# Kernel tuning notes

Measured on AMD Instinct MI355X. Metric: run time of the kernel, lower is better.

## Reference

```python
import jax, jax.numpy as jnp
import numpy as np

DIM = 192
HEADS = 6
WIN = 7


def conv2d(x, w, b, pad):
    # x: (N,C,H,W), w: (O,I,kh,kw)
    y = jax.lax.conv_general_dilated(
        x, w, window_strides=(1, 1), padding=[(pad, pad), (pad, pad)],
        dimension_numbers=('NCHW', 'OIHW', 'NCHW'))
    return y + b[None, :, None, None]


def setup_inputs() -> dict:
    key = jax.random.key(0)
    ks = jax.random.split(key, 4)
    B, C, H, W = 8, DIM, 128, 128
    D = C // HEADS
    s = lambda fan_in: 1.0 / np.sqrt(fan_in)
    return {
        'x': jax.random.normal(ks[0], (B, C, H, W), jnp.float32),
        'w_qkv': jax.random.normal(ks[1], (3 * C, C, 1, 1), jnp.float32) * s(C),
        'b_qkv': jnp.zeros((3 * C,), jnp.float32),
        'w_attn': jax.random.normal(ks[2], (WIN * WIN, 2 * D, WIN, WIN), jnp.float32) * s(2 * D * WIN * WIN),
        'b_attn': jnp.zeros((WIN * WIN,), jnp.float32),
        'w_proj': jax.random.normal(ks[3], (C, C, 1, 1), jnp.float32) * s(C),
        'b_proj': jnp.zeros((C,), jnp.float32),
    }


def reference(x, w_qkv, b_qkv, w_attn, b_attn, w_proj, b_proj):
    B, C, H, W = x.shape
    D = C // HEADS
    scale = D ** -0.5
    # qkv 1x1 conv -> (B, 3, heads, D, H, W)
    qkv = conv2d(x, w_qkv, b_qkv, 0).reshape(B, 3, HEADS, D, H, W)
    q, v = qkv[:, 0], qkv[:, 2]  # NOTE: original code uses q twice (not k)
    q_flat = q.reshape(B * HEADS, D, H, W)
    qq = jnp.concatenate([q_flat * scale, q_flat], axis=1)  # (B*heads, 2D, H, W)
    # conv-generated local attention logits over winSize^2 positions
    attn = conv2d(qq, w_attn, b_attn, WIN // 2)
    attn = jax.nn.softmax(attn, axis=1).reshape(B, HEADS, WIN * WIN, H, W)
    # sum over window dim of v (broadcast over k) * attn (broadcast over d)
    out = jnp.einsum('bhkxy,bhdxy->bhdxy', attn, v).reshape(B, C, H, W)
    return conv2d(out, w_proj, b_proj, 0)
```

## Files before the change

### kernel.cpp

```cpp
#include <hip/hip_runtime.h>
#include <stdint.h>
#include <stddef.h>


#define CDIM 192
#define HWPX 16384
#define LDS_STRIDE 200

typedef __attribute__((ext_vector_type(8))) short short8;
typedef __attribute__((ext_vector_type(4))) float floatx4;
typedef __attribute__((ext_vector_type(4))) unsigned short ushort4_t;

__device__ __forceinline__ unsigned short f2bf(float f) {
    union { float f; unsigned int u; } v; v.f = f;
    unsigned int r = (v.u + 0x7FFFu + ((v.u >> 16) & 1u)) >> 16;
    return (unsigned short)r;
}

__global__ __launch_bounds__(192) void prep_kernel(
    const float* __restrict__ w_qkv, const float* __restrict__ b_qkv,
    const float* __restrict__ w_proj, const float* __restrict__ b_proj,
    unsigned short* __restrict__ Mb, float* __restrict__ bias)
{
    const int o = blockIdx.x, c = threadIdx.x;
    const float* wpr = w_proj + o * CDIM;
    const float* wv  = w_qkv + 2 * CDIM * CDIM;
    float acc = 0.f;
    #pragma unroll 32
    for (int k = 0; k < CDIM; ++k)
        acc = fmaf(wpr[k], wv[k * CDIM + c], acc);
    Mb[o * CDIM + c] = f2bf(acc);

    __shared__ float red[CDIM];
    red[c] = wpr[c] * b_qkv[2 * CDIM + c];
    __syncthreads();
    if (c < 64) {
        float v = red[c] + red[c + 64] + red[c + 128];
        #pragma unroll
        for (int off = 32; off > 0; off >>= 1) v += __shfl_down(v, off);
        if (c == 0) bias[o] = v + b_proj[o];
    }
}

__global__ __launch_bounds__(256, 2) void fused_kernel(
    const float* __restrict__ x,
    const unsigned short* __restrict__ Mb,
    const float* __restrict__ bias,
    float* __restrict__ out)
{
    __shared__ unsigned short Xl[64 * LDS_STRIDE];

    const int tid = threadIdx.x;
    const int bid = blockIdx.x;
    const int b   = bid >> 8;
    const int p0  = (bid & 255) << 6;

    const int lane = tid & 63;
    const int w    = tid >> 6;
    const int n    = lane & 15;
    const int q    = lane >> 4;

    const float* xb = x + (size_t)b * CDIM * HWPX + p0;
    #pragma unroll
    for (int it = 0; it < 3; ++it) {
        const int slot = it * 256 + tid;
        const int p4   = slot & 15;
        const int cg4  = slot >> 4;
        const float* src = xb + (size_t)(cg4 * 4) * HWPX + p4 * 4;
        floatx4 f0 = *(const floatx4*)(src);
        floatx4 f1 = *(const floatx4*)(src + HWPX);
        floatx4 f2 = *(const floatx4*)(src + 2 * HWPX);
        floatx4 f3 = *(const floatx4*)(src + 3 * HWPX);
        #pragma unroll
        for (int i = 0; i < 4; ++i) {
            ushort4_t v4;
            v4.x = f2bf(f0[i]); v4.y = f2bf(f1[i]);
            v4.z = f2bf(f2[i]); v4.w = f2bf(f3[i]);
            *(ushort4_t*)&Xl[(p4 * 4 + i) * LDS_STRIDE + cg4 * 4] = v4;
        }
    }
    __syncthreads();

    floatx4 acc[3][4];
    #pragma unroll
    for (int t = 0; t < 3; ++t)
        #pragma unroll
        for (int pt = 0; pt < 4; ++pt)
            acc[t][pt] = (floatx4){0.f, 0.f, 0.f, 0.f};

    #pragma unroll
    for (int t = 0; t < 3; ++t) {
        const int ot = w * 3 + t;
        short8 a[6];
        const unsigned short* arow = Mb + (ot * 16 + n) * CDIM + q * 8;
        #pragma unroll
        for (int ks = 0; ks < 6; ++ks)
            a[ks] = *(const short8*)(arow + ks * 32);
        #pragma unroll
        for (int pt = 0; pt < 4; ++pt) {
            const unsigned short* brow = &Xl[(pt * 16 + n) * LDS_STRIDE + q * 8];
            #pragma unroll
            for (int ks = 0; ks < 6; ++ks) {
                short8 bfr = *(const short8*)(brow + ks * 32);
                acc[t][pt] = __builtin_amdgcn_mfma_f32_16x16x32_bf16(
                    a[ks], bfr, acc[t][pt], 0, 0, 0);
            }
        }
    }

    float* ob = out + (size_t)b * CDIM * HWPX + p0;
    #pragma unroll
    for (int t = 0; t < 3; ++t) {
        const int ot = w * 3 + t;
        #pragma unroll
        for (int r = 0; r < 4; ++r) {
            const int o = ot * 16 + q * 4 + r;
            const float bo = bias[o];
            float* orow = ob + (size_t)o * HWPX + n;
            #pragma unroll
            for (int pt = 0; pt < 4; ++pt)
                orow[pt * 16] = acc[t][pt][r] + bo;
        }
    }
}

extern "C" void kernel_launch(void* const* d_in, const int* in_sizes, int n_in,
                              void* d_out, int out_size, void* d_ws, size_t ws_size,
                              hipStream_t stream) {
    const float* x      = (const float*)d_in[0];
    const float* w_qkv  = (const float*)d_in[1];
    const float* b_qkv  = (const float*)d_in[2];
    const float* w_proj = (const float*)d_in[5];
    const float* b_proj = (const float*)d_in[6];
    float* out = (float*)d_out;

    unsigned short* Mb = (unsigned short*)d_ws;
    float* bias = (float*)((char*)d_ws + CDIM * CDIM * sizeof(unsigned short));

    const int B = in_sizes[0] / (CDIM * HWPX);

    prep_kernel<<<CDIM, CDIM, 0, stream>>>(w_qkv, b_qkv, w_proj, b_proj, Mb, bias);
    fused_kernel<<<B * 256, 256, 0, stream>>>(x, Mb, bias, out);
}
```

Baseline: 203.4 us.

## Store X in MFMA fragment layout and split work across 8 waves

The fused GEMM kernel now stages x in LDS directly in the MFMA B-fragment order, so each lane reads one short8 with no padded-stride addressing. The block doubles to 512 threads, and the 8 waves split the 64-pixel tile into 2 pixel halves by 4 output-channel groups, each holding all A fragments in registers. The global load pattern changes to per-lane strided scalar loads across channels, which may be less coalesced than the old float4 loads. The prep kernel also gains four independent accumulators to break the FMA dependency chain.

```diff
diff --git a/kernel.cpp b/kernel.cpp
--- a/kernel.cpp
+++ b/kernel.cpp
@@ -5,16 +5,13 @@
 
 #define CDIM 192
 #define HWPX 16384
-#define LDS_STRIDE 200
 
 typedef __attribute__((ext_vector_type(8))) short short8;
 typedef __attribute__((ext_vector_type(4))) float floatx4;
-typedef __attribute__((ext_vector_type(4))) unsigned short ushort4_t;
 
 __device__ __forceinline__ unsigned short f2bf(float f) {
     union { float f; unsigned int u; } v; v.f = f;
-    unsigned int r = (v.u + 0x7FFFu + ((v.u >> 16) & 1u)) >> 16;
-    return (unsigned short)r;
+    return (unsigned short)((v.u + 0x7FFFu + ((v.u >> 16) & 1u)) >> 16);
 }
 
 __global__ __launch_bounds__(192) void prep_kernel(
@@ -25,11 +22,15 @@
     const int o = blockIdx.x, c = threadIdx.x;
     const float* wpr = w_proj + o * CDIM;
     const float* wv  = w_qkv + 2 * CDIM * CDIM;
-    float acc = 0.f;
-    #pragma unroll 32
-    for (int k = 0; k < CDIM; ++k)
-        acc = fmaf(wpr[k], wv[k * CDIM + c], acc);
-    Mb[o * CDIM + c] = f2bf(acc);
+    float a0 = 0.f, a1 = 0.f, a2 = 0.f, a3 = 0.f;
+    #pragma unroll 12
+    for (int k = 0; k < CDIM; k += 4) {
+        a0 = fmaf(wpr[k + 0], wv[(k + 0) * CDIM + c], a0);
+        a1 = fmaf(wpr[k + 1], wv[(k + 1) * CDIM + c], a1);
+        a2 = fmaf(wpr[k + 2], wv[(k + 2) * CDIM + c], a2);
+        a3 = fmaf(wpr[k + 3], wv[(k + 3) * CDIM + c], a3);
+    }
+    Mb[o * CDIM + c] = f2bf((a0 + a1) + (a2 + a3));
 
     __shared__ float red[CDIM];
     red[c] = wpr[c] * b_qkv[2 * CDIM + c];
@@ -42,84 +43,83 @@
     }
 }
 
-__global__ __launch_bounds__(256, 2) void fused_kernel(
+__global__ __launch_bounds__(512, 4) void fused_kernel(
     const float* __restrict__ x,
     const unsigned short* __restrict__ Mb,
     const float* __restrict__ bias,
     float* __restrict__ out)
 {
-    __shared__ unsigned short Xl[64 * LDS_STRIDE];
+    __shared__ short8 Xl[24 * 64];
 
-    const int tid = threadIdx.x;
-    const int bid = blockIdx.x;
-    const int b   = bid >> 8;
-    const int p0  = (bid & 255) << 6;
+    const int tid  = threadIdx.x;
+    const int bid  = blockIdx.x;
+    const int b    = bid >> 8;
+    const int p0   = (bid & 255) << 6;
 
     const int lane = tid & 63;
-    const int w    = tid >> 6;
+    const int wv8  = tid >> 6;
     const int n    = lane & 15;
     const int q    = lane >> 4;
 
     const float* xb = x + (size_t)b * CDIM * HWPX + p0;
     #pragma unroll
-    for (int it = 0; it < 3; ++it) {
-        const int slot = it * 256 + tid;
-        const int p4   = slot & 15;
-        const int cg4  = slot >> 4;
-        const float* src = xb + (size_t)(cg4 * 4) * HWPX + p4 * 4;
-        floatx4 f0 = *(const floatx4*)(src);
-        floatx4 f1 = *(const floatx4*)(src + HWPX);
-        floatx4 f2 = *(const floatx4*)(src + 2 * HWPX);
-        floatx4 f3 = *(const floatx4*)(src + 3 * HWPX);
+    for (int i = 0; i < 3; ++i) {
+        const int f  = i * 8 + wv8;
+        const int pt = f / 6, ks = f % 6;
+        const float* src = xb + (size_t)(ks * 32 + q * 8) * HWPX + (pt * 16 + n);
+        float v[8];
         #pragma unroll
-        for (int i = 0; i < 4; ++i) {
-            ushort4_t v4;
-            v4.x = f2bf(f0[i]); v4.y = f2bf(f1[i]);
-            v4.z = f2bf(f2[i]); v4.w = f2bf(f3[i]);
-            *(ushort4_t*)&Xl[(p4 * 4 + i) * LDS_STRIDE + cg4 * 4] = v4;
-        }
+        for (int j = 0; j < 8; ++j) v[j] = src[(size_t)j * HWPX];
+        short8 fr;
+        #pragma unroll
+        for (int j = 0; j < 8; ++j) fr[j] = (short)f2bf(v[j]);
+        Xl[f * 64 + lane] = fr;
     }
     __syncthreads();
 
-    floatx4 acc[3][4];
+    const int w2 = wv8 & 3;
+    const int wp = wv8 >> 2;
+
+    short8 a[3][6];
+    #pragma unroll
+    for (int t = 0; t < 3; ++t) {
+        const unsigned short* ab = Mb + (size_t)((w2 * 3 + t) * 16 + n) * CDIM + q * 8;
+        #pragma unroll
+        for (int ks = 0; ks < 6; ++ks)
+            a[t][ks] = *(const short8*)(ab + ks * 32);
+    }
+
+    floatx4 acc[3][2];
     #pragma unroll
     for (int t = 0; t < 3; ++t)
         #pragma unroll
-        for (int pt = 0; pt < 4; ++pt)
-            acc[t][pt] = (floatx4){0.f, 0.f, 0.f, 0.f};
+        for (int ph = 0; ph < 2; ++ph)
+            acc[t][ph] = (floatx4){0.f, 0.f, 0.f, 0.f};
 
     #pragma unroll
-    for (int t = 0; t < 3; ++t) {
-        const int ot = w * 3 + t;
-        short8 a[6];
-        const unsigned short* arow = Mb + (ot * 16 + n) * CDIM + q * 8;
+    for (int ph = 0; ph < 2; ++ph) {
+        const int pt = wp * 2 + ph;
         #pragma unroll
-        for (int ks = 0; ks < 6; ++ks)
-            a[ks] = *(const short8*)(arow + ks * 32);
-        #pragma unroll
-        for (int pt = 0; pt < 4; ++pt) {
-            const unsigned short* brow = &Xl[(pt * 16 + n) * LDS_STRIDE + q * 8];
+        for (int ks = 0; ks < 6; ++ks) {
+            short8 bf = Xl[(pt * 6 + ks) * 64 + lane];
             #pragma unroll
-            for (int ks = 0; ks < 6; ++ks) {
-                short8 bfr = *(const short8*)(brow + ks * 32);
-                acc[t][pt] = __builtin_amdgcn_mfma_f32_16x16x32_bf16(
-                    a[ks], bfr, acc[t][pt], 0, 0, 0);
-            }
+            for (int t = 0; t < 3; ++t)
+                acc[t][ph] = __builtin_amdgcn_mfma_f32_16x16x32_bf16(
+                    a[t][ks], bf, acc[t][ph], 0, 0, 0);
         }
     }
 
     float* ob = out + (size_t)b * CDIM * HWPX + p0;
     #pragma unroll
     for (int t = 0; t < 3; ++t) {
-        const int ot = w * 3 + t;
         #pragma unroll
         for (int r = 0; r < 4; ++r) {
-            const int o = ot * 16 + q * 4 + r;
+            const int o = (w2 * 3 + t) * 16 + q * 4 + r;
             const float bo = bias[o];
             float* orow = ob + (size_t)o * HWPX + n;
             #pragma unroll
-            for (int pt = 0; pt < 4; ++pt)
-                orow[pt * 16] = acc[t][pt][r] + bo;
+            for (int ph = 0; ph < 2; ++ph)
+                orow[(wp * 2 + ph) * 16] = acc[t][ph][r] + bo;
         }
     }
 }
@@ -140,5 +140,5 @@
     const int B = in_sizes[0] / (CDIM * HWPX);
 
     prep_kernel<<<CDIM, CDIM, 0, stream>>>(w_qkv, b_qkv, w_proj, b_proj, Mb, bias);
-    fused_kernel<<<B * 256, 256, 0, stream>>>(x, Mb, bias, out);
+    fused_kernel<<<B * 256, 512, 0, stream>>>(x, Mb, bias, out);
 }
```

Measured after the change: 219.7 us. +8.0%, slower.
